# Performance work log

Hardware: AMD Instinct MI355X
Metric: run time of the kernel (lower is better)

## Reference

```python
import jax, jax.numpy as jnp
import numpy as np

N, T0, T1, C = 65536, 128, 64, 16
MIN_NEAR = 0.05


def _searchsorted(a, v):
    # batched right-side searchsorted over last dim
    return jax.vmap(lambda aa, vv: jnp.searchsorted(aa, vv, side='right'))(a, v)


def contract(x):
    # MERF-style contraction, x: [..., 3]
    ax = jnp.abs(x)
    mag = jnp.max(ax, axis=-1, keepdims=True)              # [..., 1]
    idx = jnp.argmax(ax, axis=-1)                          # [...]
    oh = jnp.arange(x.shape[-1]) == idx[..., None]         # one-hot of max axis
    inv = 1.0 / mag
    scale = jnp.where(oh, (2.0 - inv) * inv, inv)
    return jnp.where(mag < 1.0, x, x * scale)


def sample_pdf(bins, weights, T):
    # bins: [N, T0+1], weights: [N, T0] -> new bins [N, T]
    n, t0 = weights.shape
    w = weights + 0.01
    pdf = w / jnp.sum(w, -1, keepdims=True)
    cdf = jnp.minimum(jnp.cumsum(pdf, -1), 1.0)
    cdf = jnp.concatenate([jnp.zeros_like(cdf[..., :1]), cdf], -1)  # [N, T0+1]
    u = jnp.linspace(0.5 / T, 1.0 - 0.5 / T, T, dtype=bins.dtype)
    u = jnp.broadcast_to(u, (n, T))
    inds = _searchsorted(cdf, u)
    below = jnp.clip(inds - 1, 0, t0)
    above = jnp.clip(inds, 0, t0)
    g = lambda a, i: jnp.take_along_axis(a, i, axis=-1)
    cdf0, cdf1 = g(cdf, below), g(cdf, above)
    b0, b1 = g(bins, below), g(bins, above)
    t = jnp.clip(jnp.nan_to_num((u - cdf0) / (cdf1 - cdf0)), 0.0, 1.0)
    return b0 + t * (b1 - b0)


def compute_weights(real_bins, sigmas):
    deltas = real_bins[..., 1:] - real_bins[..., :-1]
    ds = deltas * sigmas
    alphas = 1.0 - jnp.exp(-ds)
    trans = jnp.exp(-jnp.concatenate(
        [jnp.zeros_like(ds[..., :1]), jnp.cumsum(ds[..., :-1], -1)], -1))
    return jnp.nan_to_num(alphas * trans)


def loss_interlevel(t0, w0, t1, w1):
    cw1 = jnp.concatenate([jnp.zeros_like(w1[..., :1]), jnp.cumsum(w1, -1)], -1)
    hi_clip = w1.shape[-1] - 1
    inds_lo = jnp.clip(_searchsorted(t1[..., :-1], t0[..., :-1]) - 1, 0, hi_clip)
    inds_hi = jnp.clip(_searchsorted(t1[..., 1:], t0[..., 1:]), 0, hi_clip)
    cw1_lo = jnp.take_along_axis(cw1[..., :-1], inds_lo, axis=-1)
    cw1_hi = jnp.take_along_axis(cw1[..., 1:], inds_hi, axis=-1)
    w = cw1_hi - cw1_lo
    return jnp.maximum(w0 - w, 0.0) ** 2 / (w0 + 1e-8)


def eff_distloss(w, m, interval):
    # efficient O(T) distortion loss (torch_efficient_distloss)
    loss_uni = (1.0 / 3.0) * jnp.mean(jnp.sum(interval * w ** 2, -1))
    wm = w * m
    w_cs = jnp.cumsum(w, -1)
    wm_cs = jnp.cumsum(wm, -1)
    loss_bi = 2.0 * jnp.mean(jnp.sum(
        wm[..., 1:] * w_cs[..., :-1] - w[..., 1:] * wm_cs[..., :-1], -1))
    return loss_uni + loss_bi


def setup_inputs():
    key = jax.random.key(0)
    ks = jax.random.split(key, 8)
    rays_o = 0.1 * jax.random.normal(ks[0], (N, 3), jnp.float32)
    rd = jax.random.normal(ks[1], (N, 3), jnp.float32)
    rays_d = rd / jnp.linalg.norm(rd, axis=-1, keepdims=True)
    aabb = jnp.array([-2.0, -2.0, -2.0, 2.0, 2.0, 2.0], jnp.float32)
    sigmas_coarse = 5.0 * jax.random.uniform(ks[2], (N, T0), jnp.float32)
    sigmas_fine = 5.0 * jax.random.uniform(ks[3], (N, T1), jnp.float32)
    colors = jax.random.uniform(ks[4], (N, T1, C), jnp.float32)
    w_view = 0.1 * jax.random.normal(ks[5], (C, 3), jnp.float32)
    b_view = jnp.zeros((3,), jnp.float32)
    return dict(rays_o=rays_o, rays_d=rays_d, aabb=aabb,
                sigmas_coarse=sigmas_coarse, sigmas_fine=sigmas_fine,
                colors=colors, w_view=w_view, b_view=b_view)


def reference(rays_o, rays_d, aabb, sigmas_coarse, sigmas_fine, colors, w_view, b_view):
    # near/far from aabb
    tmin = (aabb[:3] - rays_o) / (rays_d + 1e-15)
    tmax = (aabb[3:] - rays_o) / (rays_d + 1e-15)
    near = jnp.max(jnp.minimum(tmin, tmax), -1, keepdims=True)
    far = jnp.min(jnp.maximum(tmin, tmax), -1, keepdims=True)
    bad = far < near
    near = jnp.maximum(jnp.where(bad, 1e9, near), MIN_NEAR)
    far = jnp.where(bad, 1e9, far)

    spacing = lambda x: jnp.where(x < 1.0, x / 2.0, 1.0 - 1.0 / (2.0 * x))
    spacing_inv = lambda x: jnp.where(x < 0.5, 2.0 * x, 1.0 / (2.0 - 2.0 * x))
    s_near, s_far = spacing(near), spacing(far)

    # coarse (proposal) level: uniform bins in warped space
    bins0 = jnp.broadcast_to(jnp.linspace(0.0, 1.0, T0 + 1, dtype=rays_o.dtype), (N, T0 + 1))
    real_bins0 = spacing_inv(s_near * (1.0 - bins0) + s_far * bins0)
    weights0 = compute_weights(real_bins0, sigmas_coarse)

    # fine level: inverse-CDF sampling (detached in original)
    bins1 = sample_pdf(jax.lax.stop_gradient(bins0),
                       jax.lax.stop_gradient(weights0), T1 + 1)
    real_bins1 = spacing_inv(s_near * (1.0 - bins1) + s_far * bins1)
    rays_t = 0.5 * (real_bins1[..., 1:] + real_bins1[..., :-1])      # [N, T1]
    xyzs = rays_o[:, None, :] + rays_d[:, None, :] * rays_t[..., None]
    xyzs = contract(xyzs)                                            # [N, T1, 3]
    weights1 = compute_weights(real_bins1, sigmas_fine)

    weights_sum = jnp.sum(weights1, -1)                              # [N]
    depth = jnp.sum(weights1 * rays_t, -1)                           # [N]
    f_image = jnp.sum(weights1[..., None] * colors, -2)              # [N, C]
    image = jax.nn.sigmoid(f_image @ w_view + b_view)                # [N, 3]
    image = image + (1.0 - weights_sum)[:, None] * 1.0               # bg_color = 1
    f_xyz = jnp.sum(weights1[..., None] * xyzs, -2)                  # [N, 3]

    prop_loss = jnp.mean(loss_interlevel(
        jax.lax.stop_gradient(bins1), jax.lax.stop_gradient(weights1),
        bins0, weights0))
    intervals = bins1[..., 1:] - bins1[..., :-1]
    mids = bins1[..., :-1] + intervals / 2.0
    dist_loss = eff_distloss(weights1, mids, intervals)

    return image, depth, f_xyz, prop_loss, dist_loss
```

## Files before the change

### kernel.cpp

```cpp
#include <hip/hip_runtime.h>
#include <math.h>

#define NRAYS 65536
#define T0N 128
#define T1N 64
#define CN 16
#define RPB 4
#define NBLK (NRAYS / RPB)

#define IMG_OFF   0
#define DEPTH_OFF (NRAYS * 3)
#define FXYZ_OFF  (NRAYS * 4)
#define PROP_OFF  (NRAYS * 7)
#define DIST_OFF  (NRAYS * 7 + 1)

__device__ __forceinline__ float frcp(float x) { return __builtin_amdgcn_rcpf(x); }

template <int CTRL, int RM, int BM, bool BC>
__device__ __forceinline__ float dpp_add(float x) {
  int t = __builtin_amdgcn_update_dpp(0, __float_as_int(x), CTRL, RM, BM, BC);
  return x + __int_as_float(t);
}

__device__ __forceinline__ float scan_incl(float x) {
  x = dpp_add<0x111, 0xF, 0xF, true>(x);
  x = dpp_add<0x112, 0xF, 0xF, true>(x);
  x = dpp_add<0x114, 0xF, 0xF, true>(x);
  x = dpp_add<0x118, 0xF, 0xF, true>(x);
  x = dpp_add<0x142, 0xA, 0xF, false>(x);
  x = dpp_add<0x143, 0xC, 0xF, false>(x);
  return x;
}

__device__ __forceinline__ float reduce_hi(float x) {
  x = dpp_add<0xB1, 0xF, 0xF, true>(x);
  x = dpp_add<0x4E, 0xF, 0xF, true>(x);
  x = dpp_add<0x141, 0xF, 0xF, true>(x);
  x = dpp_add<0x140, 0xF, 0xF, true>(x);
  x = dpp_add<0x142, 0xA, 0xF, false>(x);
  x = dpp_add<0x143, 0xC, 0xF, false>(x);
  return x;
}

__device__ __forceinline__ float rl63(float x) {
  return __int_as_float(__builtin_amdgcn_readlane(__float_as_int(x), 63));
}

__device__ __forceinline__ void wave_lds_sync() {
  __builtin_amdgcn_wave_barrier();
  __builtin_amdgcn_fence(__ATOMIC_ACQ_REL, "workgroup");
  __builtin_amdgcn_wave_barrier();
}

__device__ __forceinline__ float spacing_fn(float x) {
  return (x < 1.0f) ? (x * 0.5f) : (1.0f - 0.5f * frcp(x));
}
__device__ __forceinline__ float spacing_inv_fn(float x) {
  return (x < 0.5f) ? (2.0f * x) : frcp(2.0f - 2.0f * x);
}

template <int W0>
__device__ __forceinline__ int count_le(const float* a, float v) {
  int pos = 0;
#pragma unroll
  for (int w = W0; w > 0; w >>= 1) pos += (a[pos + w - 1] <= v) ? w : 0;
  return pos;
}

__global__ void __launch_bounds__(256) nerf_main(
    const float* __restrict__ rays_o, const float* __restrict__ rays_d,
    const float* __restrict__ aabb, const float* __restrict__ sig_c,
    const float* __restrict__ sig_f, const float* __restrict__ colors,
    const float* __restrict__ w_view, const float* __restrict__ b_view,
    float* __restrict__ out, float* __restrict__ ws_partials, int use_atomic) {
  __shared__ float s_cdf[RPB][224];
  __shared__ float s_bins1[RPB][129];
  __shared__ float s_cw1[RPB][65];
  __shared__ float s_scal[RPB][2];

  const int wv = threadIdx.x >> 6;
  const int lane = threadIdx.x & 63;
  const int ray = blockIdx.x * RPB + wv;

  const int tg = lane >> 2, cg = lane & 3;
  const float4* col4 = (const float4*)(colors + (size_t)ray * (T1N * CN));
  const float4 cva = col4[(tg + 0) * 4 + cg];
  const float4 cvb = col4[(tg + 16) * 4 + cg];
  const float4 cvc = col4[(tg + 32) * 4 + cg];
  const float4 cvd = col4[(tg + 48) * 4 + cg];
  const float2 sg = ((const float2*)sig_c)[ray * 64 + lane];
  const float sgf = sig_f[ray * 64 + lane];

  float ro[3], rd[3];
#pragma unroll
  for (int c = 0; c < 3; ++c) { ro[c] = rays_o[ray * 3 + c]; rd[c] = rays_d[ray * 3 + c]; }
  float near = -3.0e38f, far = 3.0e38f;
#pragma unroll
  for (int c = 0; c < 3; ++c) {
    const float rdd = frcp(rd[c] + 1e-15f);
    float ta = (aabb[c] - ro[c]) * rdd;
    float tb = (aabb[c + 3] - ro[c]) * rdd;
    near = fmaxf(near, fminf(ta, tb));
    far = fminf(far, fmaxf(ta, tb));
  }
  if (far < near) { near = 1e9f; far = 1e9f; }
  near = fmaxf(near, 0.05f);
  const float s_near = spacing_fn(near), s_far = spacing_fn(far);

  const int i0 = 2 * lane, i1 = 2 * lane + 1;
  const float b_a = (float)i0 * (1.0f / 128.0f);
  const float b_b = (float)i1 * (1.0f / 128.0f);
  const float b_c = (float)(i1 + 1) * (1.0f / 128.0f);
  const float rb_a = spacing_inv_fn(s_near * (1.0f - b_a) + s_far * b_a);
  const float rb_b = spacing_inv_fn(s_near * (1.0f - b_b) + s_far * b_b);
  const float rb_c = spacing_inv_fn(s_near * (1.0f - b_c) + s_far * b_c);
  const float ds0 = (rb_b - rb_a) * sg.x;
  const float ds1 = (rb_c - rb_b) * sg.y;
  const float Spr = scan_incl(ds0 + ds1);
  const float E0 = Spr - (ds0 + ds1);
  const float e0 = __expf(-E0);
  const float ed0 = __expf(-ds0);
  float w00 = (1.0f - ed0) * e0;
  float w01 = (1.0f - __expf(-ds1)) * (e0 * ed0);
  if (w00 != w00) w00 = 0.0f;
  if (w01 != w01) w01 = 0.0f;

  const float wp0 = w00 + 0.01f, wp1 = w01 + 0.01f;
  const float S2 = scan_incl(wp0 + wp1);
  const float rt = frcp(rl63(S2));
  s_cdf[wv][i0 + 1] = fminf((S2 - wp1) * rt, 1.0f);
  s_cdf[wv][i1 + 1] = fminf(S2 * rt, 1.0f);
  if (lane == 0) s_cdf[wv][0] = 0.0f;
  s_cdf[wv][129 + lane] = 2.0f;
  wave_lds_sync();

  auto sample_one = [&](int j) -> float {
    const float u = ((float)j + 0.5f) * (1.0f / 65.0f);
    const int c = count_le<128>(&s_cdf[wv][0], u);
    const float c0 = s_cdf[wv][c - 1], c1 = s_cdf[wv][c];
    const float b0 = (float)(c - 1) * (1.0f / 128.0f);
    float t = (u - c0) * frcp(c1 - c0);
    t = fminf(fmaxf(t, 0.0f), 1.0f);
    const float bvv = b0 + t * (1.0f / 128.0f);
    s_bins1[wv][j] = bvv;
    return bvv;
  };
  const float bv = sample_one(lane);
  float bv64 = 0.0f;
  if (lane == 63) bv64 = sample_one(64);
  s_bins1[wv][65 + lane] = 2.0f;
  float bvn = __shfl_down(bv, 1, 64);
  if (lane == 63) bvn = bv64;

  const float rbl  = spacing_inv_fn(s_near * (1.0f - bv)  + s_far * bv);
  const float rbl1 = spacing_inv_fn(s_near * (1.0f - bvn) + s_far * bvn);
  const float dsf = (rbl1 - rbl) * sgf;
  const float Sf = scan_incl(dsf);
  float w1 = (1.0f - __expf(-dsf)) * __expf(-(Sf - dsf));
  if (w1 != w1) w1 = 0.0f;
  const float tmid = 0.5f * (rbl + rbl1);

  float px = ro[0] + rd[0] * tmid;
  float py = ro[1] + rd[1] * tmid;
  float pz = ro[2] + rd[2] * tmid;
  float cx = px, cy = py, cz = pz;
  {
    float ax = fabsf(px), ay = fabsf(py), az = fabsf(pz);
    float mag = fmaxf(ax, fmaxf(ay, az));
    if (mag >= 1.0f) {
      float inv = frcp(mag);
      float so = (2.0f - inv) * inv;
      int idx = (ax >= ay && ax >= az) ? 0 : ((ay >= az) ? 1 : 2);
      cx = px * (idx == 0 ? so : inv);
      cy = py * (idx == 1 ? so : inv);
      cz = pz * (idx == 2 ? so : inv);
    }
  }

  const float Scw = scan_incl(w1);
  const float wsum = rl63(Scw);
  const float depth_h = reduce_hi(w1 * tmid);
  const float fx_h = reduce_hi(w1 * cx);
  const float fy_h = reduce_hi(w1 * cy);
  const float fz_h = reduce_hi(w1 * cz);
  s_cw1[wv][lane + 1] = Scw;
  if (lane == 0) s_cw1[wv][0] = 0.0f;

  const float interval = bvn - bv;
  const float mid = bv + interval * 0.5f;
  const float wm = w1 * mid;
  const float Swm = scan_incl(wm);
  const float dl = (1.0f / 3.0f) * (interval * w1 * w1) +
                   2.0f * (wm * (Scw - w1) - w1 * (Swm - wm));
  const float dist_h = reduce_hi(dl);
  wave_lds_sync();

  float prop_lane = 0.0f;
  {
    const float* b1p = &s_bins1[wv][0];
    const float* cwp = &s_cw1[wv][0];
#pragma unroll
    for (int k = 0; k < 2; ++k) {
      int i = 2 * lane + k;
      float w0v = (k == 0) ? w00 : w01;
      float vlo = (float)i * (1.0f / 128.0f);
      float vhi = (float)(i + 1) * (1.0f / 128.0f);
      int ilo = max(min(count_le<64>(b1p, vlo) - 1, 63), 0);
      int ihi = min(count_le<64>(b1p + 1, vhi), 63);
      float wint = cwp[ihi + 1] - cwp[ilo];
      float diff = fmaxf(w0v - wint, 0.0f);
      prop_lane += diff * diff * frcp(w0v + 1e-8f);
    }
  }
  const float prop_h = reduce_hi(prop_lane);

  float acc0, acc1, acc2;
  {
    const float wv0 = __shfl(w1, tg, 64);
    const float wv1 = __shfl(w1, tg + 16, 64);
    const float wv2 = __shfl(w1, tg + 32, 64);
    const float wv3 = __shfl(w1, tg + 48, 64);
    const float a0 = fmaf(wv0, cva.x, fmaf(wv1, cvb.x, fmaf(wv2, cvc.x, wv3 * cvd.x)));
    const float a1 = fmaf(wv0, cva.y, fmaf(wv1, cvb.y, fmaf(wv2, cvc.y, wv3 * cvd.y)));
    const float a2 = fmaf(wv0, cva.z, fmaf(wv1, cvb.z, fmaf(wv2, cvc.z, wv3 * cvd.z)));
    const float a3 = fmaf(wv0, cva.w, fmaf(wv1, cvb.w, fmaf(wv2, cvc.w, wv3 * cvd.w)));
    const float* wvp = w_view + cg * 12;
    acc0 = reduce_hi(fmaf(a0, wvp[0], fmaf(a1, wvp[3], fmaf(a2, wvp[6], a3 * wvp[9]))));
    acc1 = reduce_hi(fmaf(a0, wvp[1], fmaf(a1, wvp[4], fmaf(a2, wvp[7], a3 * wvp[10]))));
    acc2 = reduce_hi(fmaf(a0, wvp[2], fmaf(a1, wvp[5], fmaf(a2, wvp[8], a3 * wvp[11]))));
  }

  if (lane >= 48 && lane < 51) {
    const int j = lane - 48;
    float acc = (j == 0) ? acc0 : ((j == 1) ? acc1 : acc2);
    acc += b_view[j];
    out[IMG_OFF + ray * 3 + j] = frcp(1.0f + __expf(-acc)) + (1.0f - wsum);
    out[FXYZ_OFF + ray * 3 + j] = (j == 0) ? fx_h : ((j == 1) ? fy_h : fz_h);
  }
  if (lane == 51) out[DEPTH_OFF + ray] = depth_h;
  if (lane == 52) { s_scal[wv][0] = prop_h; s_scal[wv][1] = dist_h; }
  __syncthreads();
  if (threadIdx.x == 0) {
    float P = s_scal[0][0] + s_scal[1][0] + s_scal[2][0] + s_scal[3][0];
    float D = s_scal[0][1] + s_scal[1][1] + s_scal[2][1] + s_scal[3][1];
    if (use_atomic) {
      atomicAdd(out + PROP_OFF, P * (1.0f / ((float)NRAYS * 128.0f)));
      atomicAdd(out + DIST_OFF, D * (1.0f / (float)NRAYS));
    } else {
      ws_partials[blockIdx.x] = P;
      ws_partials[NBLK + blockIdx.x] = D;
    }
  }
}

__device__ __forceinline__ float wave_sum_shfl(float x) {
#pragma unroll
  for (int off = 1; off < 64; off <<= 1) x += __shfl_xor(x, off, 64);
  return x;
}

__global__ void __launch_bounds__(256) reduce_partials(const float* __restrict__ ws,
                                                       float* __restrict__ out) {
  const float4* w4 = (const float4*)ws;
  float p = 0.0f, d = 0.0f;
  for (int i = threadIdx.x; i < NBLK / 4; i += 256) {
    float4 a = w4[i];
    p += (a.x + a.y) + (a.z + a.w);
    float4 b = w4[NBLK / 4 + i];
    d += (b.x + b.y) + (b.z + b.w);
  }
  p = wave_sum_shfl(p);
  d = wave_sum_shfl(d);
  __shared__ float sp[4], sd[4];
  const int wv = threadIdx.x >> 6, lane = threadIdx.x & 63;
  if (lane == 0) { sp[wv] = p; sd[wv] = d; }
  __syncthreads();
  if (threadIdx.x == 0) {
    float P = sp[0] + sp[1] + sp[2] + sp[3];
    float D = sd[0] + sd[1] + sd[2] + sd[3];
    out[PROP_OFF] = P * (1.0f / ((float)NRAYS * 128.0f));
    out[DIST_OFF] = D * (1.0f / (float)NRAYS);
  }
}

extern "C" void kernel_launch(void* const* d_in, const int* in_sizes, int n_in,
                              void* d_out, int out_size, void* d_ws, size_t ws_size,
                              hipStream_t stream) {
  const float* rays_o = (const float*)d_in[0];
  const float* rays_d = (const float*)d_in[1];
  const float* aabb = (const float*)d_in[2];
  const float* sig_c = (const float*)d_in[3];
  const float* sig_f = (const float*)d_in[4];
  const float* colors = (const float*)d_in[5];
  const float* w_view = (const float*)d_in[6];
  const float* b_view = (const float*)d_in[7];
  float* out = (float*)d_out;
  float* wsf = (float*)d_ws;

  const bool use_ws = (ws_size >= (size_t)(2 * NBLK) * sizeof(float)) && (wsf != nullptr);
  if (!use_ws) {
    hipMemsetAsync(out + PROP_OFF, 0, 2 * sizeof(float), stream);
  }
  nerf_main<<<NBLK, 256, 0, stream>>>(rays_o, rays_d, aabb, sig_c, sig_f, colors,
                                      w_view, b_view, out, wsf, use_ws ? 0 : 1);
  if (use_ws) reduce_partials<<<1, 256, 0, stream>>>(wsf, out);
}
```

Measured before the change: 408.4 us.

## Replace binary searches with LDS histogram scans and stage colors via global_load_lds

```diff
diff --git a/kernel.cpp b/kernel.cpp
--- a/kernel.cpp
+++ b/kernel.cpp
@@ -16,6 +16,11 @@
 
 __device__ __forceinline__ float frcp(float x) { return __builtin_amdgcn_rcpf(x); }
 
+template <int CTRL, int RM, int BM, bool BC>
+__device__ __forceinline__ int dpp_add_i(int x) {
+  int t = __builtin_amdgcn_update_dpp(0, x, CTRL, RM, BM, BC);
+  return x + t;
+}
 template <int CTRL, int RM, int BM, bool BC>
 __device__ __forceinline__ float dpp_add(float x) {
   int t = __builtin_amdgcn_update_dpp(0, __float_as_int(x), CTRL, RM, BM, BC);
@@ -31,7 +36,15 @@
   x = dpp_add<0x143, 0xC, 0xF, false>(x);
   return x;
 }
-
+__device__ __forceinline__ int scan_incl_i(int x) {
+  x = dpp_add_i<0x111, 0xF, 0xF, true>(x);
+  x = dpp_add_i<0x112, 0xF, 0xF, true>(x);
+  x = dpp_add_i<0x114, 0xF, 0xF, true>(x);
+  x = dpp_add_i<0x118, 0xF, 0xF, true>(x);
+  x = dpp_add_i<0x142, 0xA, 0xF, false>(x);
+  x = dpp_add_i<0x143, 0xC, 0xF, false>(x);
+  return x;
+}
 __device__ __forceinline__ float reduce_hi(float x) {
   x = dpp_add<0xB1, 0xF, 0xF, true>(x);
   x = dpp_add<0x4E, 0xF, 0xF, true>(x);
@@ -41,9 +54,8 @@
   x = dpp_add<0x143, 0xC, 0xF, false>(x);
   return x;
 }
-
-__device__ __forceinline__ float rl63(float x) {
-  return __int_as_float(__builtin_amdgcn_readlane(__float_as_int(x), 63));
+__device__ __forceinline__ float rlane(float x, int l) {
+  return __int_as_float(__builtin_amdgcn_readlane(__float_as_int(x), l));
 }
 
 __device__ __forceinline__ void wave_lds_sync() {
@@ -59,37 +71,50 @@
   return (x < 0.5f) ? (2.0f * x) : frcp(2.0f - 2.0f * x);
 }
 
-template <int W0>
-__device__ __forceinline__ int count_le(const float* a, float v) {
-  int pos = 0;
-#pragma unroll
-  for (int w = W0; w > 0; w >>= 1) pos += (a[pos + w - 1] <= v) ? w : 0;
-  return pos;
-}
-
-__global__ void __launch_bounds__(256) nerf_main(
+__device__ __forceinline__ int ubucket(float c) {
+  int k = (int)ceilf(fmaf(65.0f, c, -0.5f));
+  k = max(0, min(k, 65));
+  if (k > 0 && c <= ((float)(k - 1) + 0.5f) * (1.0f / 65.0f)) k -= 1;
+  else if (k < 65 && !(c <= ((float)k + 0.5f) * (1.0f / 65.0f))) k += 1;
+  return k;
+}
+
+__global__ void __launch_bounds__(256, 4) nerf_main(
     const float* __restrict__ rays_o, const float* __restrict__ rays_d,
     const float* __restrict__ aabb, const float* __restrict__ sig_c,
     const float* __restrict__ sig_f, const float* __restrict__ colors,
     const float* __restrict__ w_view, const float* __restrict__ b_view,
     float* __restrict__ out, float* __restrict__ ws_partials, int use_atomic) {
-  __shared__ float s_cdf[RPB][224];
-  __shared__ float s_bins1[RPB][129];
-  __shared__ float s_cw1[RPB][65];
+  __shared__ float s_cdf[RPB][132];
+  __shared__ float s_cw1[RPB][68];
+  __shared__ int   s_hu[RPB][68];
+  __shared__ int   s_hi[RPB][132];
+  __shared__ __align__(16) float s_col[RPB][1024];
   __shared__ float s_scal[RPB][2];
 
   const int wv = threadIdx.x >> 6;
   const int lane = threadIdx.x & 63;
   const int ray = blockIdx.x * RPB + wv;
-
   const int tg = lane >> 2, cg = lane & 3;
-  const float4* col4 = (const float4*)(colors + (size_t)ray * (T1N * CN));
-  const float4 cva = col4[(tg + 0) * 4 + cg];
-  const float4 cvb = col4[(tg + 16) * 4 + cg];
-  const float4 cvc = col4[(tg + 32) * 4 + cg];
-  const float4 cvd = col4[(tg + 48) * 4 + cg];
+
+  {
+    const float* gcol = colors + (size_t)ray * (T1N * CN);
+#pragma unroll
+    for (int q = 0; q < 4; ++q) {
+      __builtin_amdgcn_global_load_lds(
+          (const __attribute__((address_space(1))) void*)(gcol + q * 256 + lane * 4),
+          (__attribute__((address_space(3))) void*)(&s_col[wv][q * 256]),
+          16, 0, 0);
+    }
+  }
   const float2 sg = ((const float2*)sig_c)[ray * 64 + lane];
   const float sgf = sig_f[ray * 64 + lane];
+
+  s_hu[wv][lane] = 0;
+  if (lane < 4) s_hu[wv][64 + lane] = 0;
+  s_hi[wv][2 * lane] = 0;
+  s_hi[wv][2 * lane + 1] = 0;
+  if (lane < 4) s_hi[wv][128 + lane] = 0;
 
   float ro[3], rd[3];
 #pragma unroll
@@ -106,6 +131,7 @@
   if (far < near) { near = 1e9f; far = 1e9f; }
   near = fmaxf(near, 0.05f);
   const float s_near = spacing_fn(near), s_far = spacing_fn(far);
+  wave_lds_sync();
 
   const int i0 = 2 * lane, i1 = 2 * lane + 1;
   const float b_a = (float)i0 * (1.0f / 128.0f);
@@ -127,30 +153,42 @@
 
   const float wp0 = w00 + 0.01f, wp1 = w01 + 0.01f;
   const float S2 = scan_incl(wp0 + wp1);
-  const float rt = frcp(rl63(S2));
-  s_cdf[wv][i0 + 1] = fminf((S2 - wp1) * rt, 1.0f);
-  s_cdf[wv][i1 + 1] = fminf(S2 * rt, 1.0f);
+  const float rt = frcp(rlane(S2, 63));
+  const float cdf_o = fminf((S2 - wp1) * rt, 1.0f);
+  const float cdf_e = fminf(S2 * rt, 1.0f);
+  s_cdf[wv][i0 + 1] = cdf_o;
+  s_cdf[wv][i1 + 1] = cdf_e;
   if (lane == 0) s_cdf[wv][0] = 0.0f;
-  s_cdf[wv][129 + lane] = 2.0f;
+  atomicAdd(&s_hu[wv][ubucket(cdf_o)], 1);
+  atomicAdd(&s_hu[wv][ubucket(cdf_e)], 1);
   wave_lds_sync();
 
-  auto sample_one = [&](int j) -> float {
-    const float u = ((float)j + 0.5f) * (1.0f / 65.0f);
-    const int c = count_le<128>(&s_cdf[wv][0], u);
+  const int hu_l = s_hu[wv][lane];
+  const int h64 = s_hu[wv][64];
+  const int Su = scan_incl_i(hu_l);
+  auto interp = [&](int c, float u) -> float {
+    c = min(c, 128);
     const float c0 = s_cdf[wv][c - 1], c1 = s_cdf[wv][c];
-    const float b0 = (float)(c - 1) * (1.0f / 128.0f);
     float t = (u - c0) * frcp(c1 - c0);
     t = fminf(fmaxf(t, 0.0f), 1.0f);
-    const float bvv = b0 + t * (1.0f / 128.0f);
-    s_bins1[wv][j] = bvv;
-    return bvv;
+    return (float)(c - 1) * (1.0f / 128.0f) + t * (1.0f / 128.0f);
   };
-  const float bv = sample_one(lane);
-  float bv64 = 0.0f;
-  if (lane == 63) bv64 = sample_one(64);
-  s_bins1[wv][65 + lane] = 2.0f;
+  const float bv = interp(1 + Su, ((float)lane + 0.5f) * (1.0f / 65.0f));
+  float bv64s = 0.0f;
+  if (lane == 63) bv64s = interp(1 + Su + h64, 64.5f * (1.0f / 65.0f));
   float bvn = __shfl_down(bv, 1, 64);
-  if (lane == 63) bvn = bv64;
+  if (lane == 63) bvn = bv64s;
+
+  {
+    int ki = (int)ceilf(bv * 128.0f);
+    ki = max(0, min(ki, 129));
+    atomicAdd(&s_hi[wv][ki], 1);
+    if (lane == 63) {
+      int k2 = (int)ceilf(bv64s * 128.0f);
+      k2 = max(0, min(k2, 129));
+      atomicAdd(&s_hi[wv][k2], 1);
+    }
+  }
 
   const float rbl  = spacing_inv_fn(s_near * (1.0f - bv)  + s_far * bv);
   const float rbl1 = spacing_inv_fn(s_near * (1.0f - bvn) + s_far * bvn);
@@ -178,7 +216,7 @@
   }
 
   const float Scw = scan_incl(w1);
-  const float wsum = rl63(Scw);
+  const float wsum = rlane(Scw, 63);
   const float depth_h = reduce_hi(w1 * tmid);
   const float fx_h = reduce_hi(w1 * cx);
   const float fy_h = reduce_hi(w1 * cy);
@@ -197,16 +235,25 @@
 
   float prop_lane = 0.0f;
   {
-    const float* b1p = &s_bins1[wv][0];
+    const int ha = s_hi[wv][2 * lane];
+    const int hb = s_hi[wv][2 * lane + 1];
+    const int hc = s_hi[wv][2 * lane + 2];
+    const int C1 = scan_incl_i(ha + hb);
+    const int C0 = C1 - hb;
+    const int C2 = C1 + hc;
+    const float b1_0 = rlane(bv, 0);
+    const float b1_64 = rlane(bv64s, 63);
     const float* cwp = &s_cw1[wv][0];
 #pragma unroll
     for (int k = 0; k < 2; ++k) {
-      int i = 2 * lane + k;
-      float w0v = (k == 0) ? w00 : w01;
-      float vlo = (float)i * (1.0f / 128.0f);
-      float vhi = (float)(i + 1) * (1.0f / 128.0f);
-      int ilo = max(min(count_le<64>(b1p, vlo) - 1, 63), 0);
-      int ihi = min(count_le<64>(b1p + 1, vhi), 63);
+      const int i = 2 * lane + k;
+      const float w0v = (k == 0) ? w00 : w01;
+      const float vlo = (float)i * (1.0f / 128.0f);
+      const float vhi = (float)(i + 1) * (1.0f / 128.0f);
+      const int Ci = (k == 0) ? C0 : C1;
+      const int Ci1 = (k == 0) ? C1 : C2;
+      int ilo = min(max(Ci - (b1_64 <= vlo ? 1 : 0) - 1, 0), 63);
+      int ihi = min(max(Ci1 - (b1_0 <= vhi ? 1 : 0), 0), 63);
       float wint = cwp[ihi + 1] - cwp[ilo];
       float diff = fmaxf(w0v - wint, 0.0f);
       prop_lane += diff * diff * frcp(w0v + 1e-8f);
@@ -214,8 +261,15 @@
   }
   const float prop_h = reduce_hi(prop_lane);
 
+  __builtin_amdgcn_s_waitcnt(0x0F70);
+  __builtin_amdgcn_wave_barrier();
   float acc0, acc1, acc2;
   {
+    const float* cb = &s_col[wv][0];
+    const float4 cva = *(const float4*)(cb + (tg + 0) * 16 + cg * 4);
+    const float4 cvb = *(const float4*)(cb + (tg + 16) * 16 + cg * 4);
+    const float4 cvc = *(const float4*)(cb + (tg + 32) * 16 + cg * 4);
+    const float4 cvd = *(const float4*)(cb + (tg + 48) * 16 + cg * 4);
     const float wv0 = __shfl(w1, tg, 64);
     const float wv1 = __shfl(w1, tg + 16, 64);
     const float wv2 = __shfl(w1, tg + 32, 64);
```

After: 409.7 us. About the same (+0.3%).
